# Kernel tuning notes

Hardware: AMD Instinct MI355X
Metric: run time of the kernel (lower is better)

The kernel has to match this reference:

```python
import jax, jax.numpy as jnp
import numpy as np

R_CUT = 3.0  # CosineCutoff(3.0) from ANI.__init__


def cosine_cutoff(r):
    # 0.5*(cos(pi*r/rc)+1) for r < rc, else 0
    return 0.5 * (jnp.cos(jnp.pi * r / R_CUT) + 1.0) * (r < R_CUT).astype(r.dtype)


def setup_inputs() -> dict:
    key = jax.random.key(0)
    k1, k2, k3, k4 = jax.random.split(key, 4)
    B, A, N, R = 16, 2048, 96, 16
    # pair distances in [0, 4): some pairs beyond the 3.0 cutoff
    r_ij = jax.random.uniform(k1, (B, A, N), dtype=jnp.float32) * 4.0
    mask = (jax.random.uniform(k2, (B, A, N)) < 0.75).astype(jnp.float32)
    # learned parameters: etas ~ U[0.5, 1.5), rss ~ N(0,1) (matching torch defaults,
    # with rss length fixed to n_radius)
    etas = jax.random.uniform(k3, (R,), dtype=jnp.float32) + 0.5
    rss = jax.random.normal(k4, (R,), dtype=jnp.float32)
    return {"r_ij": r_ij, "mask": mask, "etas": etas, "rss": rss}


def reference(r_ij, mask, etas, rss):
    # x: [B, A, N, R] Gaussian RBF exponent
    x = -etas[None, None, None, :] * (r_ij[..., None] - rss[None, None, None, :]) ** 2
    cut = cosine_cutoff(r_ij)[..., None]          # [B, A, N, 1]
    f = jnp.exp(x) * cut * mask[..., None]        # [B, A, N, R]
    return jnp.sum(f, axis=2)                     # [B, A, R]
```

## Files before the change

kernel.cpp:

```cpp
#include <hip/hip_runtime.h>


#define NROWS 16
#define NN    96
#define RR    16
#define LP    100

__global__ __launch_bounds__(256) void ani_radial_kernel(
    const float* __restrict__ r_ij,
    const float* __restrict__ mask,
    const float* __restrict__ etas,
    const float* __restrict__ rss,
    float* __restrict__ out)
{
    __shared__ float ls_r[NROWS * LP];
    __shared__ float ls_w[NROWS * LP];

    const int tid = threadIdx.x;
    const long long rowBase = (long long)blockIdx.x * NROWS;
    const float* __restrict__ src_r = r_ij + rowBase * NN;
    const float* __restrict__ src_m = mask + rowBase * NN;

    const float PI_3 = 1.0471975511965976f;
    #pragma unroll
    for (int i = tid; i < (NROWS * NN) / 4; i += 256) {
        const int row = i / (NN / 4);
        const int nq  = i - row * (NN / 4);
        const float4 r4 = reinterpret_cast<const float4*>(src_r)[i];
        const float4 m4 = reinterpret_cast<const float4*>(src_m)[i];

        float rr[4] = {r4.x, r4.y, r4.z, r4.w};
        float mm[4] = {m4.x, m4.y, m4.z, m4.w};
        float ww[4];
        #pragma unroll
        for (int j = 0; j < 4; ++j) {
            float c = __cosf(rr[j] * PI_3);
            float w = __builtin_fmaf(0.5f, c, 0.5f);
            ww[j] = (rr[j] < 3.0f) ? w * mm[j] : 0.0f;
        }

        const int lidx = row * LP + nq * 4;
        *reinterpret_cast<float4*>(&ls_r[lidx]) = r4;
        *reinterpret_cast<float4*>(&ls_w[lidx]) =
            make_float4(ww[0], ww[1], ww[2], ww[3]);
    }
    __syncthreads();

    const int rl   = tid >> 4;
    const int rIdx = tid & 15;

    const float eta = etas[rIdx];
    const float rs  = rss[rIdx];
    const float LOG2E = 1.4426950408889634f;
    const float k  = -eta * LOG2E;
    const float pb = -2.0f * k * rs;
    const float pc = k * rs * rs;

    const float* __restrict__ lr = &ls_r[rl * LP];
    const float* __restrict__ lw = &ls_w[rl * LP];

    float acc0 = 0.0f, acc1 = 0.0f, acc2 = 0.0f, acc3 = 0.0f;
    #pragma unroll 8
    for (int nq = 0; nq < NN / 4; ++nq) {
        const float4 r4 = *reinterpret_cast<const float4*>(&lr[nq * 4]);
        const float4 w4 = *reinterpret_cast<const float4*>(&lw[nq * 4]);
        acc0 = __builtin_fmaf(
            __builtin_amdgcn_exp2f(__builtin_fmaf(__builtin_fmaf(k, r4.x, pb), r4.x, pc)),
            w4.x, acc0);
        acc1 = __builtin_fmaf(
            __builtin_amdgcn_exp2f(__builtin_fmaf(__builtin_fmaf(k, r4.y, pb), r4.y, pc)),
            w4.y, acc1);
        acc2 = __builtin_fmaf(
            __builtin_amdgcn_exp2f(__builtin_fmaf(__builtin_fmaf(k, r4.z, pb), r4.z, pc)),
            w4.z, acc2);
        acc3 = __builtin_fmaf(
            __builtin_amdgcn_exp2f(__builtin_fmaf(__builtin_fmaf(k, r4.w, pb), r4.w, pc)),
            w4.w, acc3);
    }

    const float acc = (acc0 + acc1) + (acc2 + acc3);
    out[(rowBase + rl) * RR + rIdx] = acc;
}

extern "C" void kernel_launch(void* const* d_in, const int* in_sizes, int n_in,
                              void* d_out, int out_size, void* d_ws, size_t ws_size,
                              hipStream_t stream) {
    const float* r_ij = (const float*)d_in[0];
    const float* mask = (const float*)d_in[1];
    const float* etas = (const float*)d_in[2];
    const float* rss  = (const float*)d_in[3];
    float* out = (float*)d_out;

    const int totalRows = in_sizes[0] / NN;
    const int grid = totalRows / NROWS;

    ani_radial_kernel<<<grid, 256, 0, stream>>>(r_ij, mask, etas, rss, out);
}
```

Baseline: 14.12 us.

## Replace LDS staging with per-thread neighbor split and shuffle transpose-reduction

Removes the shared-memory staging and barrier. Each 16-lane group now reads one row's distances and masks directly from global memory, six neighbors per lane, and computes the cutoff weight once per neighbor. Each lane accumulates all 16 radial terms in registers, then a butterfly shuffle reduce-scatter leaves each lane holding one radial output. This removes LDS traffic and the barrier at the cost of more registers and float2 rather than float4 loads. It also uses the hardware cos builtin, which takes its input in revolutions, hence the 1/6 scale.

```diff
diff --git a/kernel.cpp b/kernel.cpp
--- a/kernel.cpp
+++ b/kernel.cpp
@@ -1,10 +1,8 @@
 #include <hip/hip_runtime.h>
 
 
-#define NROWS 16
-#define NN    96
-#define RR    16
-#define LP    100
+#define NN 96
+#define RR 16
 
 __global__ __launch_bounds__(256) void ani_radial_kernel(
     const float* __restrict__ r_ij,
@@ -13,73 +11,70 @@
     const float* __restrict__ rss,
     float* __restrict__ out)
 {
-    __shared__ float ls_r[NROWS * LP];
-    __shared__ float ls_w[NROWS * LP];
+    const int tid  = threadIdx.x;
+    const int rowL = tid >> 4;
+    const int t    = tid & 15;
+    const long long row = (long long)blockIdx.x * 16 + rowL;
 
-    const int tid = threadIdx.x;
-    const long long rowBase = (long long)blockIdx.x * NROWS;
-    const float* __restrict__ src_r = r_ij + rowBase * NN;
-    const float* __restrict__ src_m = mask + rowBase * NN;
-
-    const float PI_3 = 1.0471975511965976f;
+    const float LOG2E = 1.4426950408889634f;
+    float k[RR], pb[RR], pc[RR];
     #pragma unroll
-    for (int i = tid; i < (NROWS * NN) / 4; i += 256) {
-        const int row = i / (NN / 4);
-        const int nq  = i - row * (NN / 4);
-        const float4 r4 = reinterpret_cast<const float4*>(src_r)[i];
-        const float4 m4 = reinterpret_cast<const float4*>(src_m)[i];
-
-        float rr[4] = {r4.x, r4.y, r4.z, r4.w};
-        float mm[4] = {m4.x, m4.y, m4.z, m4.w};
-        float ww[4];
-        #pragma unroll
-        for (int j = 0; j < 4; ++j) {
-            float c = __cosf(rr[j] * PI_3);
-            float w = __builtin_fmaf(0.5f, c, 0.5f);
-            ww[j] = (rr[j] < 3.0f) ? w * mm[j] : 0.0f;
-        }
-
-        const int lidx = row * LP + nq * 4;
-        *reinterpret_cast<float4*>(&ls_r[lidx]) = r4;
-        *reinterpret_cast<float4*>(&ls_w[lidx]) =
-            make_float4(ww[0], ww[1], ww[2], ww[3]);
-    }
-    __syncthreads();
-
-    const int rl   = tid >> 4;
-    const int rIdx = tid & 15;
-
-    const float eta = etas[rIdx];
-    const float rs  = rss[rIdx];
-    const float LOG2E = 1.4426950408889634f;
-    const float k  = -eta * LOG2E;
-    const float pb = -2.0f * k * rs;
-    const float pc = k * rs * rs;
-
-    const float* __restrict__ lr = &ls_r[rl * LP];
-    const float* __restrict__ lw = &ls_w[rl * LP];
-
-    float acc0 = 0.0f, acc1 = 0.0f, acc2 = 0.0f, acc3 = 0.0f;
-    #pragma unroll 8
-    for (int nq = 0; nq < NN / 4; ++nq) {
-        const float4 r4 = *reinterpret_cast<const float4*>(&lr[nq * 4]);
-        const float4 w4 = *reinterpret_cast<const float4*>(&lw[nq * 4]);
-        acc0 = __builtin_fmaf(
-            __builtin_amdgcn_exp2f(__builtin_fmaf(__builtin_fmaf(k, r4.x, pb), r4.x, pc)),
-            w4.x, acc0);
-        acc1 = __builtin_fmaf(
-            __builtin_amdgcn_exp2f(__builtin_fmaf(__builtin_fmaf(k, r4.y, pb), r4.y, pc)),
-            w4.y, acc1);
-        acc2 = __builtin_fmaf(
-            __builtin_amdgcn_exp2f(__builtin_fmaf(__builtin_fmaf(k, r4.z, pb), r4.z, pc)),
-            w4.z, acc2);
-        acc3 = __builtin_fmaf(
-            __builtin_amdgcn_exp2f(__builtin_fmaf(__builtin_fmaf(k, r4.w, pb), r4.w, pc)),
-            w4.w, acc3);
+    for (int r = 0; r < RR; ++r) {
+        const float eta = etas[r];
+        const float rs  = rss[r];
+        k[r]  = -eta * LOG2E;
+        pb[r] = -2.0f * k[r] * rs;
+        pc[r] = k[r] * rs * rs;
     }
 
-    const float acc = (acc0 + acc1) + (acc2 + acc3);
-    out[(rowBase + rl) * RR + rIdx] = acc;
+    const float* __restrict__ pr = r_ij + row * NN;
+    const float* __restrict__ pm = mask + row * NN;
+
+    float acc[RR];
+    #pragma unroll
+    for (int r = 0; r < RR; ++r) acc[r] = 0.0f;
+
+    float dd[6], mm[6];
+    #pragma unroll
+    for (int j = 0; j < 3; ++j) {
+        const int n = 32 * j + 2 * t;
+        const float2 d2 = *reinterpret_cast<const float2*>(pr + n);
+        const float2 m2 = *reinterpret_cast<const float2*>(pm + n);
+        dd[2*j]   = d2.x; dd[2*j+1] = d2.y;
+        mm[2*j]   = m2.x; mm[2*j+1] = m2.y;
+    }
+
+    #pragma unroll
+    for (int u = 0; u < 6; ++u) {
+        const float d = dd[u];
+        const float c = __builtin_amdgcn_cosf(d * 0.16666666666666666f);
+        float w = __builtin_fmaf(0.5f, c, 0.5f);
+        w = (d < 3.0f) ? w * mm[u] : 0.0f;
+        #pragma unroll
+        for (int r = 0; r < RR; ++r) {
+            const float e = __builtin_fmaf(__builtin_fmaf(k[r], d, pb[r]), d, pc[r]);
+            acc[r] = __builtin_fmaf(__builtin_amdgcn_exp2f(e), w, acc[r]);
+        }
+    }
+
+#define RSTAGE(S, NV)                                                   \
+    {                                                                   \
+        const bool hi = (t & (S)) != 0;                                 \
+        _Pragma("unroll")                                               \
+        for (int i = 0; i < (NV) / 2; ++i) {                            \
+            const float send = hi ? acc[i] : acc[i + (NV) / 2];         \
+            const float recv = __shfl_xor(send, (S), 16);               \
+            const float keep = hi ? acc[i + (NV) / 2] : acc[i];         \
+            acc[i] = keep + recv;                                       \
+        }                                                               \
+    }
+    RSTAGE(8, 16)
+    RSTAGE(4, 8)
+    RSTAGE(2, 4)
+    RSTAGE(1, 2)
+#undef RSTAGE
+
+    out[row * RR + t] = acc[0];
 }
 
 extern "C" void kernel_launch(void* const* d_in, const int* in_sizes, int n_in,
@@ -92,7 +87,7 @@
     float* out = (float*)d_out;
 
     const int totalRows = in_sizes[0] / NN;
-    const int grid = totalRows / NROWS;
+    const int grid = totalRows / 16;
 
     ani_radial_kernel<<<grid, 256, 0, stream>>>(r_ij, mask, etas, rss, out);
 }
```

New measurement: 15.30 us. +8.4%, slower.
